# Performance work log

Measured on AMD Instinct MI355X. Metric: run time of the kernel, lower is better.

Reference implementation:

```python
import jax, jax.numpy as jnp
import numpy as np

F_DIM = 128; T = 3; N_RBF = 20; CUTOFF = 5.0; EPS = 1e-8
N_ATOMS = 10000; N_EDGES = 320000; N_MOL = 16; MAX_Z = 100


def setup_inputs():
    key = jax.random.key(0)
    ks = jax.random.split(key, 30)
    def w(k, shape, fan_in):
        return (jax.random.normal(k, shape, dtype=jnp.float32) / np.float32(np.sqrt(fan_in)))
    inp = {}
    inp["atomic_numbers"] = jax.random.randint(ks[0], (N_ATOMS,), 1, MAX_Z)
    inp["r_ij"] = jax.random.normal(ks[1], (N_EDGES, 3), dtype=jnp.float32) * 1.5
    inp["idx_i"] = jax.random.randint(ks[2], (N_EDGES,), 0, N_ATOMS)
    inp["idx_j"] = jax.random.randint(ks[3], (N_EDGES,), 0, N_ATOMS)
    inp["idx_m"] = jnp.sort(jax.random.randint(ks[4], (N_ATOMS,), 0, N_MOL))
    inp["e_field"] = jax.random.normal(ks[5], (N_MOL, 3), dtype=jnp.float32) * 0.1
    emb = jax.random.normal(ks[6], (MAX_Z, F_DIM), dtype=jnp.float32)
    inp["emb"] = emb.at[0].set(0.0)  # padding_idx=0
    inp["filt_W"] = w(ks[7], (N_RBF, T * 3 * F_DIM), N_RBF)
    inp["filt_b"] = jnp.zeros((T * 3 * F_DIM,), jnp.float32)
    inp["inter_W1"] = w(ks[8], (T, F_DIM, F_DIM), F_DIM)
    inp["inter_b1"] = jnp.zeros((T, F_DIM), jnp.float32)
    inp["inter_W2"] = w(ks[9], (T, F_DIM, 3 * F_DIM), F_DIM)
    inp["inter_b2"] = jnp.zeros((T, 3 * F_DIM), jnp.float32)
    inp["field_sW1"] = w(ks[10], (T, F_DIM, F_DIM), F_DIM)
    inp["field_sb1"] = jnp.zeros((T, F_DIM), jnp.float32)
    inp["field_sW2"] = w(ks[11], (T, F_DIM, F_DIM), F_DIM)
    inp["field_sb2"] = jnp.zeros((T, F_DIM), jnp.float32)
    inp["field_vW"] = w(ks[12], (T, F_DIM, F_DIM), F_DIM)
    inp["mix_muW"] = w(ks[13], (T, F_DIM, 2 * F_DIM), F_DIM)
    inp["mix_W1"] = w(ks[14], (T, 2 * F_DIM, F_DIM), 2 * F_DIM)
    inp["mix_b1"] = jnp.zeros((T, F_DIM), jnp.float32)
    inp["mix_W2"] = w(ks[15], (T, F_DIM, 3 * F_DIM), F_DIM)
    inp["mix_b2"] = jnp.zeros((T, 3 * F_DIM), jnp.float32)
    return inp


def _forward(r_ij, e_field, emb, filt_W, filt_b, inter_W1, inter_b1, inter_W2, inter_b2,
             field_sW1, field_sb1, field_sW2, field_sb2, field_vW,
             mix_muW, mix_W1, mix_b1, mix_W2, mix_b2,
             atomic_numbers, idx_i, idx_j, idx_m):
    silu = jax.nn.silu
    n_atoms = atomic_numbers.shape[0]
    # distances / directions
    d = jnp.sqrt(jnp.sum(r_ij * r_ij, axis=1, keepdims=True))        # [E,1]
    dir_ij = r_ij / d                                                # [E,3]
    # Gaussian RBF expansion
    offsets = jnp.linspace(0.0, CUTOFF, N_RBF, dtype=jnp.float32)
    width = offsets[1] - offsets[0]
    phi = jnp.exp(-0.5 * ((d[..., None] - offsets) / width) ** 2)    # [E,1,n_rbf]
    # cosine cutoff
    fcut = 0.5 * (jnp.cos(d * jnp.pi / CUTOFF) + 1.0) * (d < CUTOFF) # [E,1]
    filters = (phi @ filt_W + filt_b) * fcut[..., None]              # [E,1,T*3F]
    filter_list = jnp.split(filters, T, axis=-1)                     # T x [E,1,3F]
    q = emb[atomic_numbers][:, None, :]                              # [N,1,F]
    mu = jnp.zeros((n_atoms, 3, F_DIM), dtype=q.dtype)               # [N,3,F]
    E = e_field[idx_m][..., None]                                    # [N,3,1]
    for t in range(T):
        # --- PaiNNInteraction: edge message passing ---
        x = silu(q @ inter_W1[t] + inter_b1[t]) @ inter_W2[t] + inter_b2[t]  # [N,1,3F]
        xj = x[idx_j]                                                # [E,1,3F]
        muj = mu[idx_j]                                              # [E,3,F]
        xx = filter_list[t] * xj                                     # [E,1,3F]
        dq_e, dmuR, dmumu = jnp.split(xx, 3, axis=-1)                # [E,1,F] each
        dq = jax.ops.segment_sum(dq_e[:, 0, :], idx_i, num_segments=n_atoms)[:, None, :]
        dmu_e = dmuR * dir_ij[:, :, None] + dmumu * muj              # [E,3,F]
        dmu = jax.ops.segment_sum(dmu_e, idx_i, num_segments=n_atoms)
        q = q + dq
        mu = mu + dmu
        # --- FieldInteraction: pseudo-polarizability coupling ---
        a_s = silu(q @ field_sW1[t] + field_sb1[t]) @ field_sW2[t] + field_sb2[t]  # [N,1,F]
        a_v = mu @ field_vW[t]                                       # [N,3,F]
        mu = mu + a_s * E - jnp.sum(a_v * E, axis=1, keepdims=True) * a_v
        # --- PaiNNMixing: intra-atomic scalar/vector mixing ---
        mu_mix = mu @ mix_muW[t]                                     # [N,3,2F]
        mu_V, mu_Wc = jnp.split(mu_mix, 2, axis=-1)                  # [N,3,F]
        mu_Vn = jnp.sqrt(jnp.sum(mu_V ** 2, axis=-2, keepdims=True) + EPS)  # [N,1,F]
        ctx = jnp.concatenate([q, mu_Vn], axis=-1)                   # [N,1,2F]
        y = silu(ctx @ mix_W1[t] + mix_b1[t]) @ mix_W2[t] + mix_b2[t]  # [N,1,3F]
        dq_i, dmu_i, dqmu_i = jnp.split(y, 3, axis=-1)
        q = q + dq_i + dqmu_i * jnp.sum(mu_V * mu_Wc, axis=1, keepdims=True)
        mu = mu + dmu_i * mu_Wc
    # pack scalar (q [N,1,F]) and vector (mu [N,3,F]) reps into [N,4,F]
    return jnp.concatenate([q, mu], axis=1)


def reference(atomic_numbers, r_ij, idx_i, idx_j, idx_m, e_field, emb, filt_W, filt_b,
              inter_W1, inter_b1, inter_W2, inter_b2,
              field_sW1, field_sb1, field_sW2, field_sb2, field_vW,
              mix_muW, mix_W1, mix_b1, mix_W2, mix_b2):
    return _forward(r_ij, e_field, emb, filt_W, filt_b, inter_W1, inter_b1, inter_W2, inter_b2,
                    field_sW1, field_sb1, field_sW2, field_sb2, field_vW,
                    mix_muW, mix_W1, mix_b1, mix_W2, mix_b2,
                    atomic_numbers, idx_i, idx_j, idx_m)
```

## Files before the change

### kernel.cpp

```cpp
#include <hip/hip_runtime.h>

#define NA 10000
#define NE 320000

typedef short short8 __attribute__((ext_vector_type(8)));
typedef unsigned short us4 __attribute__((ext_vector_type(4)));
typedef float f32x4 __attribute__((ext_vector_type(4)));

__device__ __forceinline__ float silu_f(float v) { return v / (1.0f + __expf(-v)); }

__device__ __forceinline__ void split_bf16(float x, unsigned short& h, unsigned short& l)
{
    unsigned int u = __float_as_uint(x);
    h = (unsigned short)(u >> 16);
    float hf = __uint_as_float((unsigned int)h << 16);
    unsigned int ul = __float_as_uint(x - hf) + 0x8000u;
    l = (unsigned short)(ul >> 16);
}

__global__ __launch_bounds__(256) void k_init(
    const int* __restrict__ Z, const int* __restrict__ idx_m,
    const float* __restrict__ emb, const float* __restrict__ e_field,
    float* __restrict__ q, float* __restrict__ mu,
    float* __restrict__ Eat, int* __restrict__ counts, int* __restrict__ cursor)
{
    int gid = blockIdx.x * 256 + threadIdx.x;
    if (gid < NA * 384) mu[gid] = 0.0f;
    if (gid < NA * 128) {
        int i = gid >> 7, f = gid & 127;
        q[gid] = emb[Z[i] * 128 + f];
    }
    if (gid < NA * 3) {
        int i = gid / 3, d = gid - i * 3;
        Eat[gid] = e_field[idx_m[i] * 3 + d];
    }
    if (gid < NA) { counts[gid] = 0; cursor[gid] = 0; }
}

__global__ __launch_bounds__(256) void k_count(
    const int* __restrict__ idx_i, int* __restrict__ counts)
{
    int e = blockIdx.x * 256 + threadIdx.x;
    if (e < NE) atomicAdd(&counts[idx_i[e]], 1);
}

__global__ __launch_bounds__(256) void k_scan(const int* __restrict__ counts,
                                              int* __restrict__ rowptr)
{
    __shared__ int part[256];
    int tid = threadIdx.x;
    const int CH = (NA + 255) / 256;
    int base = tid * CH;
    int s = 0;
    for (int i2 = 0; i2 < CH; i2++) {
        int idx = base + i2;
        if (idx < NA) s += counts[idx];
    }
    part[tid] = s;
    __syncthreads();
    for (int ofs = 1; ofs < 256; ofs <<= 1) {
        int v = part[tid];
        int add = (tid >= ofs) ? part[tid - ofs] : 0;
        __syncthreads();
        part[tid] = v + add;
        __syncthreads();
    }
    int run = (tid > 0) ? part[tid - 1] : 0;
    for (int i2 = 0; i2 < CH; i2++) {
        int idx = base + i2;
        if (idx < NA) { rowptr[idx] = run; run += counts[idx]; }
        else if (idx == NA) rowptr[NA] = run;
    }
}

__global__ __launch_bounds__(256) void k_geom_scatter(
    const float* __restrict__ r_ij, const int* __restrict__ idx_i,
    const int* __restrict__ idx_j, const int* __restrict__ rowptr,
    int* __restrict__ cursor, float* __restrict__ phi_s,
    float4* __restrict__ df_s, int* __restrict__ j_s)
{
    int e = blockIdx.x * 256 + threadIdx.x;
    if (e >= NE) return;
    float x = r_ij[e*3+0], y = r_ij[e*3+1], z = r_ij[e*3+2];
    float d = sqrtf(x*x + y*y + z*z);
    float inv = 1.0f / d;
    float fc = (d < 5.0f) ? 0.5f * (__cosf(d * 0.628318530717958648f) + 1.0f) : 0.0f;
    int i = idx_i[e];
    int pos = rowptr[i] + atomicAdd(&cursor[i], 1);
    float4 dv; dv.x = x*inv; dv.y = y*inv; dv.z = z*inv; dv.w = fc;
    df_s[pos] = dv;
    j_s[pos] = idx_j[e];
    const float invw = 19.0f / 5.0f;
    float ph[20];
    #pragma unroll
    for (int k = 0; k < 20; k++) {
        float off = (5.0f / 19.0f) * (float)k;
        float u = (d - off) * invw;
        ph[k] = __expf(-0.5f * u * u) * fc;
    }
    #pragma unroll
    for (int c = 0; c < 5; c++) {
        float4 pv; pv.x = ph[c*4]; pv.y = ph[c*4+1]; pv.z = ph[c*4+2]; pv.w = ph[c*4+3];
        *(float4*)(phi_s + (size_t)pos*20 + c*4) = pv;
    }
}

struct WDesc { const float* src; unsigned short* dh; unsigned short* dl; int K; int N; };
struct WPack { WDesc w[24]; };

__global__ __launch_bounds__(256) void k_wprep(WPack P)
{
    WDesc d = P.w[blockIdx.y];
    int kBlks = d.K >> 5, nStrips = d.N >> 4;
    int total = nStrips * kBlks * 64;
    int g = blockIdx.x * 256 + threadIdx.x;
    if (g >= total) return;
    int lane = g & 63, rem = g >> 6;
    int kb = rem % kBlks, sIdx = rem / kBlks;
    int m16 = lane & 15, quad = lane >> 4;
    int n = sIdx * 16 + m16;
    int kbase = kb * 32 + quad * 8;
    size_t dofs = (size_t)g * 8;
    #pragma unroll
    for (int jj = 0; jj < 8; jj++) {
        unsigned short h, l;
        split_bf16(d.src[(size_t)(kbase + jj) * d.N + n], h, l);
        d.dh[dofs + jj] = h;
        d.dl[dofs + jj] = l;
    }
}

__global__ __launch_bounds__(256) void k_wfprep(
    const float* __restrict__ filt_W, const float* __restrict__ filt_b,
    unsigned short* __restrict__ wfh, unsigned short* __restrict__ wfl)
{
    int g = blockIdx.x * 256 + threadIdx.x;
    if (g >= 3 * 24 * 64) return;
    int lane = g & 63, rem = g >> 6;
    int st = rem % 24, t = rem / 24;
    int col = lane & 15, quad = lane >> 4;
    int tcol = t * 384 + st * 16 + col;
    size_t dofs = (size_t)g * 8;
    #pragma unroll
    for (int j = 0; j < 8; j++) {
        int k = quad * 8 + j;
        float v = 0.0f;
        if (k < 20) v = filt_W[k * 1152 + tcol];
        else if (k == 20) v = filt_b[tcol];
        unsigned short hh, ll;
        split_bf16(v, hh, ll);
        wfh[dofs + j] = hh;
        wfl[dofs + j] = ll;
    }
}

template<int ACT>
__global__ __launch_bounds__(256) void k_gmm2(
    const float* __restrict__ A,
    const unsigned short* __restrict__ Bh, const unsigned short* __restrict__ Bl,
    const float* __restrict__ bias, float* __restrict__ C,
    int M, int K, int N)
{
    __shared__ unsigned short Ahs[64 * 40];
    __shared__ unsigned short Als[64 * 40];
    int tid = threadIdx.x, lane = tid & 63, wv = tid >> 6;
    int i0 = blockIdx.x * 64, n0 = blockIdx.y * 64;
    int m16 = lane & 15, quad = lane >> 4;
    int kBlks = K >> 5;
    int sIdx = blockIdx.y * 4 + wv;

    f32x4 acc[4];
    #pragma unroll
    for (int a = 0; a < 4; a++) acc[a] = 0.0f;

    for (int kb = 0; kb < kBlks; kb++) {
        int k0 = kb << 5;
        __syncthreads();
        #pragma unroll
        for (int s = 0; s < 2; s++) {
            int idx = s * 256 + tid;
            int r = idx >> 3, c4 = (idx & 7) << 2;
            float4 v = {0.f, 0.f, 0.f, 0.f};
            if (i0 + r < M) v = *(const float4*)(A + (size_t)(i0 + r) * K + k0 + c4);
            unsigned short h0,l0,h1,l1,h2,l2,h3,l3;
            split_bf16(v.x, h0, l0); split_bf16(v.y, h1, l1);
            split_bf16(v.z, h2, l2); split_bf16(v.w, h3, l3);
            us4 hv = {h0, h1, h2, h3}, lv = {l0, l1, l2, l3};
            *(us4*)(Ahs + r * 40 + c4) = hv;
            *(us4*)(Als + r * 40 + c4) = lv;
        }
        __syncthreads();
        size_t bofs = (((size_t)sIdx * kBlks + kb) * 64 + lane) * 8;
        short8 bh = *(const short8*)(Bh + bofs);
        short8 bl = *(const short8*)(Bl + bofs);
        #pragma unroll
        for (int tm = 0; tm < 4; tm++) {
            short8 ah = *(const short8*)(Ahs + (tm * 16 + m16) * 40 + quad * 8);
            short8 al = *(const short8*)(Als + (tm * 16 + m16) * 40 + quad * 8);
            acc[tm] = __builtin_amdgcn_mfma_f32_16x16x32_bf16(ah, bh, acc[tm], 0, 0, 0);
            acc[tm] = __builtin_amdgcn_mfma_f32_16x16x32_bf16(ah, bl, acc[tm], 0, 0, 0);
            acc[tm] = __builtin_amdgcn_mfma_f32_16x16x32_bf16(al, bh, acc[tm], 0, 0, 0);
        }
    }
    int col = n0 + wv * 16 + m16;
    float bv = bias ? bias[col] : 0.0f;
    #pragma unroll
    for (int tm = 0; tm < 4; tm++) {
        #pragma unroll
        for (int r = 0; r < 4; r++) {
            int row = i0 + tm * 16 + quad * 4 + r;
            if (row < M) {
                float v = acc[tm][r] + bv;
                if (ACT) v = silu_f(v);
                C[(size_t)row * N + col] = v;
            }
        }
    }
}

template<int K1, int N2, int PRO, int EPI>
__global__ __launch_bounds__(256, 2) void k_mlp(
    const float* __restrict__ A, const float* __restrict__ mumix,
    const unsigned short* __restrict__ B1h, const unsigned short* __restrict__ B1l,
    const float* __restrict__ b1,
    const unsigned short* __restrict__ B2h, const unsigned short* __restrict__ B2l,
    const float* __restrict__ b2,
    float* __restrict__ C,
    const float* __restrict__ av, const float* __restrict__ Eat,
    float* __restrict__ qRW, float* __restrict__ muRW,
    float* __restrict__ outPk, int last, int M)
{
    const int KB1 = K1 / 32;
    const int S2  = N2 / 64;
    __shared__ unsigned short A1h[32 * 40];
    __shared__ unsigned short A1l[32 * 40];
    __shared__ unsigned short Hh[32 * 136];
    __shared__ unsigned short Hl[32 * 136];
    __shared__ float Ys[EPI == 2 ? 32 * 384 : 1];

    int tid = threadIdx.x, lane = tid & 63, wv = tid >> 6;
    int i0 = blockIdx.x * 32;
    int m16 = lane & 15, quad = lane >> 4;

    f32x4 acc1[2][2];
    #pragma unroll
    for (int s = 0; s < 2; s++)
        #pragma unroll
        for (int tm = 0; tm < 2; tm++) acc1[s][tm] = 0.0f;

    for (int kb = 0; kb < KB1; kb++) {
        int k0 = kb << 5;
        __syncthreads();
        {
            int r = tid >> 3, c4 = (tid & 7) << 2;
            int row = i0 + r;
            float4 v = {0.f, 0.f, 0.f, 0.f};
            if (row < M) {
                if (PRO == 0) {
                    v = *(const float4*)(A + (size_t)row * K1 + k0 + c4);
                } else {
                    int g = k0 + c4;
                    if (g < 128) {
                        v = *(const float4*)(A + (size_t)row * 128 + g);
                    } else {
                        int f = g - 128;
                        float4 v0 = *(const float4*)(mumix + ((size_t)row*3 + 0)*256 + f);
                        float4 v1 = *(const float4*)(mumix + ((size_t)row*3 + 1)*256 + f);
                        float4 v2 = *(const float4*)(mumix + ((size_t)row*3 + 2)*256 + f);
                        v.x = sqrtf(v0.x*v0.x + v1.x*v1.x + v2.x*v2.x + 1e-8f);
                        v.y = sqrtf(v0.y*v0.y + v1.y*v1.y + v2.y*v2.y + 1e-8f);
                        v.z = sqrtf(v0.z*v0.z + v1.z*v1.z + v2.z*v2.z + 1e-8f);
                        v.w = sqrtf(v0.w*v0.w + v1.w*v1.w + v2.w*v2.w + 1e-8f);
                    }
                }
            }
            unsigned short h0,l0,h1,l1,h2,l2,h3,l3;
            split_bf16(v.x, h0, l0); split_bf16(v.y, h1, l1);
            split_bf16(v.z, h2, l2); split_bf16(v.w, h3, l3);
            us4 hv = {h0, h1, h2, h3}, lv = {l0, l1, l2, l3};
            *(us4*)(A1h + r * 40 + c4) = hv;
            *(us4*)(A1l + r * 40 + c4) = lv;
        }
        __syncthreads();
        #pragma unroll
        for (int tm = 0; tm < 2; tm++) {
            short8 ah = *(const short8*)(A1h + (tm * 16 + m16) * 40 + quad * 8);
            short8 al = *(const short8*)(A1l + (tm * 16 + m16) * 40 + quad * 8);
            #pragma unroll
            for (int s = 0; s < 2; s++) {
                int sIdx = wv * 2 + s;
                size_t bofs = (((size_t)sIdx * KB1 + kb) * 64 + lane) * 8;
                short8 bh = *(const short8*)(B1h + bofs);
                short8 bl = *(const short8*)(B1l + bofs);
                acc1[s][tm] = __builtin_amdgcn_mfma_f32_16x16x32_bf16(ah, bh, acc1[s][tm], 0, 0, 0);
                acc1[s][tm] = __builtin_amdgcn_mfma_f32_16x16x32_bf16(ah, bl, acc1[s][tm], 0, 0, 0);
                acc1[s][tm] = __builtin_amdgcn_mfma_f32_16x16x32_bf16(al, bh, acc1[s][tm], 0, 0, 0);
            }
        }
    }
    __syncthreads();
    #pragma unroll
    for (int s = 0; s < 2; s++) {
        int col = wv * 32 + s * 16 + m16;
        float bb = b1[col];
        #pragma unroll
        for (int tm = 0; tm < 2; tm++) {
            #pragma unroll
            for (int r = 0; r < 4; r++) {
                int row = tm * 16 + quad * 4 + r;
                float v = silu_f(acc1[s][tm][r] + bb);
                unsigned short h, l;
                split_bf16(v, h, l);
                Hh[row * 136 + col] = h;
                Hl[row * 136 + col] = l;
            }
        }
    }
    __syncthreads();

    f32x4 acc2[S2][2];
    #pragma unroll
    for (int s = 0; s < S2; s++)
        #pragma unroll
        for (int tm = 0; tm < 2; tm++) acc2[s][tm] = 0.0f;

    #pragma unroll
    for (int kb = 0; kb < 4; kb++) {
        short8 ah[2], al[2];
        #pragma unroll
        for (int tm = 0; tm < 2; tm++) {
            ah[tm] = *(const short8*)(Hh + (tm * 16 + m16) * 136 + kb * 32 + quad * 8);
            al[tm] = *(const short8*)(Hl + (tm * 16 + m16) * 136 + kb * 32 + quad * 8);
        }
        #pragma unroll
        for (int s = 0; s < S2; s++) {
            int sIdx = wv * S2 + s;
            size_t bofs = (((size_t)sIdx * 4 + kb) * 64 + lane) * 8;
            short8 bh = *(const short8*)(B2h + bofs);
            short8 bl = *(const short8*)(B2l + bofs);
            #pragma unroll
            for (int tm = 0; tm < 2; tm++) {
                acc2[s][tm] = __builtin_amdgcn_mfma_f32_16x16x32_bf16(ah[tm], bh, acc2[s][tm], 0, 0, 0);
                acc2[s][tm] = __builtin_amdgcn_mfma_f32_16x16x32_bf16(ah[tm], bl, acc2[s][tm], 0, 0, 0);
                acc2[s][tm] = __builtin_amdgcn_mfma_f32_16x16x32_bf16(al[tm], bh, acc2[s][tm], 0, 0, 0);
            }
        }
    }

    if (EPI == 0) {
        #pragma unroll
        for (int s = 0; s < S2; s++) {
            int col = (wv * S2 + s) * 16 + m16;
            float bb = b2 ? b2[col] : 0.0f;
            #pragma unroll
            for (int tm = 0; tm < 2; tm++) {
                #pragma unroll
                for (int r = 0; r < 4; r++) {
                    int row = i0 + tm * 16 + quad * 4 + r;
                    if (row < M) C[(size_t)row * N2 + col] = acc2[s][tm][r] + bb;
                }
            }
        }
    } else if (EPI == 1) {
        #pragma unroll
        for (int s = 0; s < S2; s++) {
            int col = (wv * S2 + s) * 16 + m16;
            float bb = b2[col];
            #pragma unroll
            for (int tm = 0; tm < 2; tm++) {
                #pragma unroll
                for (int r = 0; r < 4; r++) {
                    int row = i0 + tm * 16 + quad * 4 + r;
                    if (row < M) {
                        float as = acc2[s][tm][r] + bb;
                        float E0 = Eat[row*3+0], E1 = Eat[row*3+1], E2 = Eat[row*3+2];
                        size_t b0 = ((size_t)row*3 + 0)*128 + col;
                        size_t b1o = ((size_t)row*3 + 1)*128 + col;
                        size_t b2o = ((size_t)row*3 + 2)*128 + col;
                        float a0 = av[b0], a1 = av[b1o], a2 = av[b2o];
                        float dot = a0*E0 + a1*E1 + a2*E2;
                        muRW[b0] += as*E0 - dot*a0;
                        muRW[b1o] += as*E1 - dot*a1;
                        muRW[b2o] += as*E2 - dot*a2;
                    }
                }
            }
        }
    } else {
        #pragma unroll
        for (int s = 0; s < S2; s++) {
            int col = (wv * S2 + s) * 16 + m16;
            float bb = b2[col];
            #pragma unroll
            for (int tm = 0; tm < 2; tm++) {
                #pragma unroll
                for (int r = 0; r < 4; r++) {
                    int row = tm * 16 + quad * 4 + r;
                    Ys[row * 384 + col] = acc2[s][tm][r] + bb;
                }
            }
        }
        __syncthreads();
        int f = tid & 127;
        #pragma unroll
        for (int it = 0; it < 16; it++) {
            int row = (tid >> 7) + it * 2;
            int i = i0 + row;
            if (i < M) {
                float yq  = Ys[row * 384 + f];
                float ym  = Ys[row * 384 + 128 + f];
                float yqm = Ys[row * 384 + 256 + f];
                float sdot = 0.0f;
                float W[3];
                #pragma unroll
                for (int d = 0; d < 3; d++) {
                    float Vd = mumix[((size_t)i*3 + d)*256 + f];
                    W[d]     = mumix[((size_t)i*3 + d)*256 + 128 + f];
                    sdot += Vd * W[d];
                }
                float qn = qRW[(size_t)i*128 + f] + yq + yqm * sdot;
                qRW[(size_t)i*128 + f] = qn;
                float mun[3];
                #pragma unroll
                for (int d = 0; d < 3; d++) {
                    size_t mo = ((size_t)i*3 + d)*128 + f;
                    mun[d] = muRW[mo] + ym * W[d];
                    muRW[mo] = mun[d];
                }
                if (last) {
                    outPk[(size_t)i*512 + f] = qn;
                    #pragma unroll
                    for (int d = 0; d < 3; d++)
                        outPk[(size_t)i*512 + 128 + d*128 + f] = mun[d];
                }
            }
        }
    }
}

__global__ __launch_bounds__(256) void k_edgeM(
    int t, const float* __restrict__ phi_s, const float4* __restrict__ df_s,
    const int* __restrict__ j_s, const int* __restrict__ rowptr,
    const float* __restrict__ x, const float* __restrict__ mu_in,
    const unsigned short* __restrict__ wfh, const unsigned short* __restrict__ wfl,
    float* __restrict__ q, float* __restrict__ mu_out)
{
    int lane = threadIdx.x & 63;
    int g  = blockIdx.x * 4 + (threadIdx.x >> 6);
    int ia = g >> 1;
    int h  = g & 1;
    int col = lane & 15, quad = lane >> 4;

    int p0 = rowptr[ia], p1 = rowptr[ia + 1];

    float accq[4] = {};
    float accd[3][4] = {};

    for (int pb = p0; pb < p1; pb += 16) {
        int e = pb + col;
        bool val = (e < p1);
        int ec = val ? e : (p1 - 1);
        float av[8] = {0,0,0,0,0,0,0,0};
        if (val) {
            const float* pr = phi_s + (size_t)ec * 20;
            if (quad == 0) {
                float4 a = *(const float4*)(pr);
                float4 b = *(const float4*)(pr + 4);
                av[0]=a.x; av[1]=a.y; av[2]=a.z; av[3]=a.w;
                av[4]=b.x; av[5]=b.y; av[6]=b.z; av[7]=b.w;
            } else if (quad == 1) {
                float4 a = *(const float4*)(pr + 8);
                float4 b = *(const float4*)(pr + 12);
                av[0]=a.x; av[1]=a.y; av[2]=a.z; av[3]=a.w;
                av[4]=b.x; av[5]=b.y; av[6]=b.z; av[7]=b.w;
            } else if (quad == 2) {
                float4 a = *(const float4*)(pr + 16);
                av[0]=a.x; av[1]=a.y; av[2]=a.z; av[3]=a.w;
                av[4]=df_s[ec].w;
            }
        }
        short8 ah, al;
        #pragma unroll
        for (int j = 0; j < 8; j++) {
            unsigned short hh, ll;
            split_bf16(av[j], hh, ll);
            ah[j] = (short)hh; al[j] = (short)ll;
        }

        f32x4 dt[3][4];
        #pragma unroll
        for (int c = 0; c < 3; c++) {
            #pragma unroll
            for (int s = 0; s < 4; s++) {
                int st = c * 8 + h * 4 + s;
                size_t bo = (((size_t)(t * 24 + st)) * 64 + lane) * 8;
                short8 bh = *(const short8*)(wfh + bo);
                short8 bl = *(const short8*)(wfl + bo);
                f32x4 d = {0.f, 0.f, 0.f, 0.f};
                d = __builtin_amdgcn_mfma_f32_16x16x32_bf16(ah, bh, d, 0, 0, 0);
                d = __builtin_amdgcn_mfma_f32_16x16x32_bf16(ah, bl, d, 0, 0, 0);
                d = __builtin_amdgcn_mfma_f32_16x16x32_bf16(al, bh, d, 0, 0, 0);
                dt[c][s] = d;
            }
        }

        #pragma unroll
        for (int r = 0; r < 4; r++) {
            int pe = pb + quad * 4 + r;
            if (pe > p1 - 1) pe = p1 - 1;
            int j = j_s[pe];
            float4 dfr = df_s[pe];
            size_t xb = (size_t)j * 384 + h * 64 + col;
            size_t mb = (size_t)j * 384 + h * 64 + col;
            #pragma unroll
            for (int s = 0; s < 4; s++) {
                int o = s * 16;
                float xq  = x[xb + o];
                float xr_ = x[xb + 128 + o];
                float xm  = x[xb + 256 + o];
                float m0  = mu_in[mb + o];
                float m1  = mu_in[mb + 128 + o];
                float m2  = mu_in[mb + 256 + o];
                accq[s]    += dt[0][s][r] * xq;
                float xxr = dt[1][s][r] * xr_;
                float xxm = dt[2][s][r] * xm;
                accd[0][s] += xxr * dfr.x + xxm * m0;
                accd[1][s] += xxr * dfr.y + xxm * m1;
                accd[2][s] += xxr * dfr.z + xxm * m2;
            }
        }
    }

    #pragma unroll
    for (int s = 0; s < 4; s++) {
        accq[s] += __shfl_xor(accq[s], 16);
        accq[s] += __shfl_xor(accq[s], 32);
        #pragma unroll
        for (int d = 0; d < 3; d++) {
            accd[d][s] += __shfl_xor(accd[d][s], 16);
            accd[d][s] += __shfl_xor(accd[d][s], 32);
        }
    }
    if (quad == 0) {
        #pragma unroll
        for (int s = 0; s < 4; s++) {
            size_t qo = (size_t)ia * 128 + h * 64 + s * 16 + col;
            q[qo] += accq[s];
            #pragma unroll
            for (int d = 0; d < 3; d++) {
                size_t mo = ((size_t)ia * 3 + d) * 128 + h * 64 + s * 16 + col;
                mu_out[mo] = mu_in[mo] + accd[d][s];
            }
        }
    }
}

extern "C" void kernel_launch(void* const* d_in, const int* in_sizes, int n_in,
                              void* d_out, int out_size, void* d_ws, size_t ws_size,
                              hipStream_t stream)
{
    const int*   Z       = (const int*)d_in[0];
    const float* r_ij    = (const float*)d_in[1];
    const int*   idx_i   = (const int*)d_in[2];
    const int*   idx_j   = (const int*)d_in[3];
    const int*   idx_m   = (const int*)d_in[4];
    const float* e_field = (const float*)d_in[5];
    const float* emb     = (const float*)d_in[6];
    const float* filt_W  = (const float*)d_in[7];
    const float* filt_b  = (const float*)d_in[8];
    const float* iW1     = (const float*)d_in[9];
    const float* ib1     = (const float*)d_in[10];
    const float* iW2     = (const float*)d_in[11];
    const float* ib2     = (const float*)d_in[12];
    const float* sW1     = (const float*)d_in[13];
    const float* sb1     = (const float*)d_in[14];
    const float* sW2     = (const float*)d_in[15];
    const float* sb2     = (const float*)d_in[16];
    const float* vW      = (const float*)d_in[17];
    const float* mmW     = (const float*)d_in[18];
    const float* mW1     = (const float*)d_in[19];
    const float* mb1     = (const float*)d_in[20];
    const float* mW2     = (const float*)d_in[21];
    const float* mb2     = (const float*)d_in[22];
    float* out = (float*)d_out;

    float* base = (float*)d_ws;
    size_t off = 0;
    auto alloc = [&](size_t n) { float* p = base + off; off += (n + 255) & ~(size_t)255; return p; };
    float* q     = alloc((size_t)NA*128);
    float* mu_a  = alloc((size_t)NA*384);
    float* mu_b  = alloc((size_t)NA*384);
    float* s384  = alloc((size_t)NA*384);
    float* mumix = alloc((size_t)NA*768);
    float* Eat   = alloc((size_t)NA*3);
    float* phi_s = alloc((size_t)NE*20);
    float4* df_s = (float4*)alloc((size_t)NE*4);
    int* rowptr  = (int*)alloc(NA + 1);
    int* counts  = (int*)alloc(NA);
    int* cursor  = (int*)alloc(NA);
    int* j_s     = (int*)alloc(NE);
    unsigned short* wth = (unsigned short*)alloc(344064 + 256);
    unsigned short* wtl = (unsigned short*)alloc(344064 + 256);
    unsigned short* wfh = (unsigned short*)alloc(3*24*64*8/2 + 256);
    unsigned short* wfl = (unsigned short*)alloc(3*24*64*8/2 + 256);
    (void)ws_size; (void)in_sizes; (void)n_in; (void)out_size;

    WPack P;
    size_t woff = 0;
    unsigned short* WH[3][8];
    unsigned short* WL[3][8];
    int nw = 0;
    auto reg = [&](const float* src, int K, int N, int t, int slot) {
        P.w[nw].src = src; P.w[nw].dh = wth + woff; P.w[nw].dl = wtl + woff;
        P.w[nw].K = K; P.w[nw].N = N;
        WH[t][slot] = wth + woff; WL[t][slot] = wtl + woff;
        woff += (size_t)K * N; nw++;
    };
    for (int t = 0; t < 3; t++) {
        reg(iW1 + t*128*128, 128, 128, t, 0);
        reg(iW2 + t*128*384, 128, 384, t, 1);
        reg(sW1 + t*128*128, 128, 128, t, 2);
        reg(sW2 + t*128*128, 128, 128, t, 3);
        reg(vW  + t*128*128, 128, 128, t, 4);
        reg(mmW + t*128*256, 128, 256, t, 5);
        reg(mW1 + t*256*128, 256, 128, t, 6);
        reg(mW2 + t*128*384, 128, 384, t, 7);
    }

    k_wprep       <<<dim3(24, 24),          256, 0, stream>>>(P);
    k_wfprep      <<<18,                    256, 0, stream>>>(filt_W, filt_b, wfh, wfl);
    k_init        <<<(NA*384 + 255)/256,    256, 0, stream>>>(Z, idx_m, emb, e_field, q, mu_a, Eat, counts, cursor);
    k_count       <<<(NE + 255)/256,        256, 0, stream>>>(idx_i, counts);
    k_scan        <<<1,                     256, 0, stream>>>(counts, rowptr);
    k_geom_scatter<<<(NE + 255)/256,        256, 0, stream>>>(r_ij, idx_i, idx_j, rowptr, cursor,
                                                              phi_s, df_s, j_s);

    const int G32   = (NA + 31) / 32;
    const int G64x3 = (NA*3 + 63) / 64;
    float* mu_cur = mu_a;
    float* mu_nxt = mu_b;
    for (int t = 0; t < 3; t++) {
        k_mlp<128,384,0,0><<<G32, 256, 0, stream>>>(
            q, nullptr, WH[t][0], WL[t][0], ib1 + t*128, WH[t][1], WL[t][1], ib2 + t*384,
            s384, nullptr, nullptr, nullptr, nullptr, nullptr, 0, NA);
        k_edgeM<<<NA/2, 256, 0, stream>>>(t, phi_s, df_s, j_s, rowptr, s384,
                                          mu_cur, wfh, wfl, q, mu_nxt);
        { float* tmp = mu_cur; mu_cur = mu_nxt; mu_nxt = tmp; }
        k_gmm2<0><<<dim3(G64x3, 2), 256, 0, stream>>>(mu_cur, WH[t][4], WL[t][4], nullptr, s384, NA*3, 128, 128);
        k_mlp<128,128,0,1><<<G32, 256, 0, stream>>>(
            q, nullptr, WH[t][2], WL[t][2], sb1 + t*128, WH[t][3], WL[t][3], sb2 + t*128,
            nullptr, s384, Eat, nullptr, mu_cur, nullptr, 0, NA);
        k_gmm2<0><<<dim3(G64x3, 4), 256, 0, stream>>>(mu_cur, WH[t][5], WL[t][5], nullptr, mumix, NA*3, 128, 256);
        k_mlp<256,384,1,2><<<G32, 256, 0, stream>>>(
            q, mumix, WH[t][6], WL[t][6], mb1 + t*128, WH[t][7], WL[t][7], mb2 + t*384,
            nullptr, nullptr, nullptr, q, mu_cur, out, (t == 2) ? 1 : 0, NA);
    }
}
```

Baseline: 1.017 ms.

## Fuse mu projection GEMMs into the following MLP kernels as a prologue

Removes the two standalone k_gmm2 launches per interaction layer (mu @ field_vW and mu @ mix_muW). Each k_mlp block now first computes the projection for its own 32 atoms (96 rows of mu) with split-bf16 MFMA, writes the result to global memory, then runs the MLP after a block barrier. This cuts six kernel launches and the separate read of mu. In exchange, the prologue reads A fragments straight from global without LDS staging and does more work per block at low grid size. It also depends on a block-local fence being enough for the MLP stage to read back the rows that block just wrote.

```diff
diff --git a/kernel.cpp b/kernel.cpp
--- a/kernel.cpp
+++ b/kernel.cpp
@@ -154,77 +154,15 @@
     }
 }
 
-template<int ACT>
-__global__ __launch_bounds__(256) void k_gmm2(
-    const float* __restrict__ A,
-    const unsigned short* __restrict__ Bh, const unsigned short* __restrict__ Bl,
-    const float* __restrict__ bias, float* __restrict__ C,
-    int M, int K, int N)
-{
-    __shared__ unsigned short Ahs[64 * 40];
-    __shared__ unsigned short Als[64 * 40];
-    int tid = threadIdx.x, lane = tid & 63, wv = tid >> 6;
-    int i0 = blockIdx.x * 64, n0 = blockIdx.y * 64;
-    int m16 = lane & 15, quad = lane >> 4;
-    int kBlks = K >> 5;
-    int sIdx = blockIdx.y * 4 + wv;
-
-    f32x4 acc[4];
-    #pragma unroll
-    for (int a = 0; a < 4; a++) acc[a] = 0.0f;
-
-    for (int kb = 0; kb < kBlks; kb++) {
-        int k0 = kb << 5;
-        __syncthreads();
-        #pragma unroll
-        for (int s = 0; s < 2; s++) {
-            int idx = s * 256 + tid;
-            int r = idx >> 3, c4 = (idx & 7) << 2;
-            float4 v = {0.f, 0.f, 0.f, 0.f};
-            if (i0 + r < M) v = *(const float4*)(A + (size_t)(i0 + r) * K + k0 + c4);
-            unsigned short h0,l0,h1,l1,h2,l2,h3,l3;
-            split_bf16(v.x, h0, l0); split_bf16(v.y, h1, l1);
-            split_bf16(v.z, h2, l2); split_bf16(v.w, h3, l3);
-            us4 hv = {h0, h1, h2, h3}, lv = {l0, l1, l2, l3};
-            *(us4*)(Ahs + r * 40 + c4) = hv;
-            *(us4*)(Als + r * 40 + c4) = lv;
-        }
-        __syncthreads();
-        size_t bofs = (((size_t)sIdx * kBlks + kb) * 64 + lane) * 8;
-        short8 bh = *(const short8*)(Bh + bofs);
-        short8 bl = *(const short8*)(Bl + bofs);
-        #pragma unroll
-        for (int tm = 0; tm < 4; tm++) {
-            short8 ah = *(const short8*)(Ahs + (tm * 16 + m16) * 40 + quad * 8);
-            short8 al = *(const short8*)(Als + (tm * 16 + m16) * 40 + quad * 8);
-            acc[tm] = __builtin_amdgcn_mfma_f32_16x16x32_bf16(ah, bh, acc[tm], 0, 0, 0);
-            acc[tm] = __builtin_amdgcn_mfma_f32_16x16x32_bf16(ah, bl, acc[tm], 0, 0, 0);
-            acc[tm] = __builtin_amdgcn_mfma_f32_16x16x32_bf16(al, bh, acc[tm], 0, 0, 0);
-        }
-    }
-    int col = n0 + wv * 16 + m16;
-    float bv = bias ? bias[col] : 0.0f;
-    #pragma unroll
-    for (int tm = 0; tm < 4; tm++) {
-        #pragma unroll
-        for (int r = 0; r < 4; r++) {
-            int row = i0 + tm * 16 + quad * 4 + r;
-            if (row < M) {
-                float v = acc[tm][r] + bv;
-                if (ACT) v = silu_f(v);
-                C[(size_t)row * N + col] = v;
-            }
-        }
-    }
-}
-
-template<int K1, int N2, int PRO, int EPI>
+template<int K1, int N2, int PRO, int EPI, int PRE>
 __global__ __launch_bounds__(256, 2) void k_mlp(
     const float* __restrict__ A, const float* __restrict__ mumix,
     const unsigned short* __restrict__ B1h, const unsigned short* __restrict__ B1l,
     const float* __restrict__ b1,
     const unsigned short* __restrict__ B2h, const unsigned short* __restrict__ B2l,
     const float* __restrict__ b2,
+    const unsigned short* __restrict__ Bgh, const unsigned short* __restrict__ Bgl,
+    float* __restrict__ Gout,
     float* __restrict__ C,
     const float* __restrict__ av, const float* __restrict__ Eat,
     float* __restrict__ qRW, float* __restrict__ muRW,
@@ -241,6 +179,58 @@
     int tid = threadIdx.x, lane = tid & 63, wv = tid >> 6;
     int i0 = blockIdx.x * 32;
     int m16 = lane & 15, quad = lane >> 4;
+
+    if (PRE > 0) {
+        const int NG  = (PRE == 1) ? 128 : 256;
+        const int SPW = NG / 64;
+        #pragma unroll
+        for (int mt = 0; mt < 6; mt++) {
+            int rowbase = i0 * 3 + mt * 16;
+            f32x4 ga[SPW];
+            #pragma unroll
+            for (int s = 0; s < SPW; s++) ga[s] = 0.0f;
+            #pragma unroll
+            for (int kb = 0; kb < 4; kb++) {
+                int arow = rowbase + m16;
+                float va[8] = {0,0,0,0,0,0,0,0};
+                if (arow < 3 * M) {
+                    const float* ap = muRW + (size_t)arow * 128 + kb * 32 + quad * 8;
+                    float4 u0 = *(const float4*)(ap);
+                    float4 u1 = *(const float4*)(ap + 4);
+                    va[0]=u0.x; va[1]=u0.y; va[2]=u0.z; va[3]=u0.w;
+                    va[4]=u1.x; va[5]=u1.y; va[6]=u1.z; va[7]=u1.w;
+                }
+                short8 ah, al;
+                #pragma unroll
+                for (int j = 0; j < 8; j++) {
+                    unsigned short hh, ll;
+                    split_bf16(va[j], hh, ll);
+                    ah[j] = (short)hh; al[j] = (short)ll;
+                }
+                #pragma unroll
+                for (int s = 0; s < SPW; s++) {
+                    int sIdx = wv * SPW + s;
+                    size_t bo = (((size_t)sIdx * 4 + kb) * 64 + lane) * 8;
+                    short8 bh = *(const short8*)(Bgh + bo);
+                    short8 bl = *(const short8*)(Bgl + bo);
+                    ga[s] = __builtin_amdgcn_mfma_f32_16x16x32_bf16(ah, bh, ga[s], 0, 0, 0);
+                    ga[s] = __builtin_amdgcn_mfma_f32_16x16x32_bf16(ah, bl, ga[s], 0, 0, 0);
+                    ga[s] = __builtin_amdgcn_mfma_f32_16x16x32_bf16(al, bh, ga[s], 0, 0, 0);
+                }
+            }
+            #pragma unroll
+            for (int s = 0; s < SPW; s++) {
+                int gcol = (wv * SPW + s) * 16 + m16;
+                #pragma unroll
+                for (int r = 0; r < 4; r++) {
+                    int grow = rowbase + quad * 4 + r;
+                    if (grow < 3 * M) Gout[(size_t)grow * NG + gcol] = ga[s][r];
+                }
+            }
+        }
+        __threadfence_block();
+        __syncthreads();
+    }
 
     f32x4 acc1[2][2];
     #pragma unroll
@@ -635,24 +625,24 @@
     k_geom_scatter<<<(NE + 255)/256,        256, 0, stream>>>(r_ij, idx_i, idx_j, rowptr, cursor,
                                                               phi_s, df_s, j_s);
 
-    const int G32   = (NA + 31) / 32;
-    const int G64x3 = (NA*3 + 63) / 64;
+    const int G32 = (NA + 31) / 32;
     float* mu_cur = mu_a;
     float* mu_nxt = mu_b;
     for (int t = 0; t < 3; t++) {
-        k_mlp<128,384,0,0><<<G32, 256, 0, stream>>>(
+        k_mlp<128,384,0,0,0><<<G32, 256, 0, stream>>>(
             q, nullptr, WH[t][0], WL[t][0], ib1 + t*128, WH[t][1], WL[t][1], ib2 + t*384,
+            nullptr, nullptr, nullptr,
             s384, nullptr, nullptr, nullptr, nullptr, nullptr, 0, NA);
         k_edgeM<<<NA/2, 256, 0, stream>>>(t, phi_s, df_s, j_s, rowptr, s384,
                                           mu_cur, wfh, wfl, q, mu_nxt);
         { float* tmp = mu_cur; mu_cur = mu_nxt; mu_nxt = tmp; }
-        k_gmm2<0><<<dim3(G64x3, 2), 256, 0, stream>>>(mu_cur, WH[t][4], WL[t][4], nullptr, s384, NA*3, 128, 128);
-        k_mlp<128,128,0,1><<<G32, 256, 0, stream>>>(
+        k_mlp<128,128,0,1,1><<<G32, 256, 0, stream>>>(
             q, nullptr, WH[t][2], WL[t][2], sb1 + t*128, WH[t][3], WL[t][3], sb2 + t*128,
+            WH[t][4], WL[t][4], s384,
             nullptr, s384, Eat, nullptr, mu_cur, nullptr, 0, NA);
-        k_gmm2<0><<<dim3(G64x3, 4), 256, 0, stream>>>(mu_cur, WH[t][5], WL[t][5], nullptr, mumix, NA*3, 128, 256);
-        k_mlp<256,384,1,2><<<G32, 256, 0, stream>>>(
+        k_mlp<256,384,1,2,2><<<G32, 256, 0, stream>>>(
             q, mumix, WH[t][6], WL[t][6], mb1 + t*128, WH[t][7], WL[t][7], mb2 + t*384,
+            WH[t][5], WL[t][5], mumix,
             nullptr, nullptr, nullptr, q, mu_cur, out, (t == 2) ? 1 : 0, NA);
     }
 }
```

New measurement: 1.007 ms. Within noise of the previous version (-1.0%).
